# Performance work log

Measured on AMD Instinct MI355X. Metric: run time of the kernel, lower is better.

The kernel has to match this reference:

```python
import jax, jax.numpy as jnp
import numpy as np

N, K, D = 1000000, 8, 32


def setup_inputs() -> dict:
    key = jax.random.key(0)
    k_x, k_mu, k_phi = jax.random.split(key, 3)
    X = jax.random.normal(k_x, (N, D), dtype=jnp.float32)
    # Gaussian.__init__: mu = (rand(dims) - 0.5) * 2, sigma = eye(dims)
    mus = (jax.random.uniform(k_mu, (K, D), dtype=jnp.float32) - 0.5) * 2.0
    sigmas = jnp.broadcast_to(jnp.eye(D, dtype=jnp.float32), (K, D, D)).copy()
    # GMM.__init__: phi ~ Dirichlet(1/count); approximate with normalized uniforms
    phi_raw = jax.random.uniform(k_phi, (K,), dtype=jnp.float32) + 1e-3
    phis = phi_raw / phi_raw.sum()
    return {"X": X, "mus": mus, "sigmas": sigmas, "phis": phis}


def reference(X, mus, sigmas, phis):
    # X: [N, D], mus: [K, D], sigmas: [K, D, D], phis: [K]
    d = X.shape[1]
    inv_sigma = jnp.linalg.pinv(sigmas)                      # [K, D, D]
    _, logdet = jnp.linalg.slogdet(sigmas)                   # [K]
    log_two_pi_dims = d * jnp.log(jnp.asarray(2.0 * np.pi, dtype=X.dtype))
    log_den = 0.5 * (log_two_pi_dims + logdet)               # [K]
    diff = X[:, None, :] - mus[None, :, :]                   # [N, K, D]
    # batched Mahalanobis quadratic form: -0.5 * diff @ inv_sigma @ diff^T (diag)
    quad = -0.5 * jnp.einsum('nkd,kde,nke->nk', diff, inv_sigma, diff)  # [N, K]
    # original subtracts exp(log_den), then scales by phi per mixture
    aff = phis[None, :] * (quad - jnp.exp(log_den)[None, :])  # [N, K]
    # ExpNormalizer.exp_norm == row-wise softmax
    return jax.nn.softmax(aff, axis=1)
```

## Files before the change

### kernel.cpp

```cpp
#include <hip/hip_runtime.h>
#include <hip/hip_bf16.h>
#include <math.h>

#define DDIM 32
#define KMIX 8
#define TPW 10

typedef short bf16x8 __attribute__((ext_vector_type(8)));
typedef float f32x4 __attribute__((ext_vector_type(4)));

__device__ __forceinline__ ushort to_bf16_rne(float f) {
    unsigned u = __builtin_bit_cast(unsigned, f);
    u = (u + 0x7FFFu + ((u >> 16) & 1u)) >> 16;
    return (ushort)u;
}

__global__ __launch_bounds__(512) void gmm_prep(
    const float* __restrict__ S, const float* __restrict__ mus,
    const float* __restrict__ phis, ushort* __restrict__ Wtg,
    ushort* __restrict__ Upan, float* __restrict__ pa2, float* __restrict__ pc)
{
    __shared__ float aug[DDIM][2 * DDIM + 2];
    __shared__ float pivsave[DDIM];
    __shared__ float irts[DDIM];
    __shared__ float wv[DDIM];
    const int k = blockIdx.x;
    const int t = threadIdx.x;
    const int r = t >> 4;
    const int c4 = t & 15;

    aug[r][c4]      = S[k * 1024 + r * 32 + c4];
    aug[r][c4 + 16] = S[k * 1024 + r * 32 + c4 + 16];
    aug[r][c4 + 32] = (c4 == r) ? 1.f : 0.f;
    aug[r][c4 + 48] = (c4 + 16 == r) ? 1.f : 0.f;
    __syncthreads();

    for (int p = 0; p < DDIM; ++p) {
        const float piv = aug[p][p];
        const float f   = aug[r][p];
        const float pr0 = aug[p][c4];
        const float pr1 = aug[p][c4 + 16];
        const float pr2 = aug[p][c4 + 32];
        const float pr3 = aug[p][c4 + 48];
        __syncthreads();
        if (r > p) {
            const float fi = f * __builtin_amdgcn_rcpf(piv);
            aug[r][c4]      = fmaf(-fi, pr0, aug[r][c4]);
            aug[r][c4 + 16] = fmaf(-fi, pr1, aug[r][c4 + 16]);
            aug[r][c4 + 32] = fmaf(-fi, pr2, aug[r][c4 + 32]);
            aug[r][c4 + 48] = fmaf(-fi, pr3, aug[r][c4 + 48]);
        }
        if (t == (p << 4)) pivsave[p] = piv;
        __syncthreads();
    }

    if (t < DDIM) irts[t] = rsqrtf(pivsave[t]);
    __syncthreads();

    if (t < DDIM) {
        float acc = 0.f;
        for (int d = 0; d <= t; ++d)
            acc = fmaf(aug[t][32 + d], mus[k * 32 + d], acc);
        wv[t] = acc * irts[t];
    }
    __syncthreads();

    if (t < DDIM) {
        float acc = 0.f;
        for (int e = t; e < DDIM; ++e)
            acc = fmaf(aug[e][32 + t] * irts[e], wv[e], acc);
        Upan[k * 32 + t] = to_bf16_rne(phis[k] * 1.4426950408889634f * acc);
    }
    if (k == 0 && t >= 256) Upan[t] = 0;

    {
        const int lane0 = (t >> 3) & 63, j0 = t & 7;
        const int d0 = (lane0 >> 4) * 8 + j0;
        const int e0 = lane0 & 15;
        const int e1 = 16 + e0;
        const float f0 = (d0 <= e0) ? aug[e0][32 + d0] * irts[e0] : 0.f;
        const float f1 = (d0 <= e1) ? aug[e1][32 + d0] * irts[e1] : 0.f;
        Wtg[k * 1024 + t]       = to_bf16_rne(f0);
        Wtg[k * 1024 + 512 + t] = to_bf16_rne(f1);
    }

    if (t < 64) {
        float l  = (t < DDIM) ? logf(pivsave[t]) : 0.f;
        float w2 = (t < DDIM) ? wv[t] * wv[t] : 0.f;
        for (int off = 32; off; off >>= 1) {
            l  += __shfl_xor(l, off, 64);
            w2 += __shfl_xor(w2, off, 64);
        }
        if (t == 0) {
            const float eld = expf(0.5f * (DDIM * 1.8378770664093453f + l));
            const float LOG2E = 1.4426950408889634f;
            pa2[k] = -0.5f * phis[k] * LOG2E;
            pc[k]  = (-0.5f * phis[k] * w2 - phis[k] * eld) * LOG2E;
        }
    }
}

template <int CTRL>
__device__ __forceinline__ float dpp_add(float v) {
    int t = __builtin_amdgcn_update_dpp(0, __builtin_bit_cast(int, v), CTRL, 0xF, 0xF, true);
    return v + __builtin_bit_cast(float, t);
}
__device__ __forceinline__ float sel4(float a0, float a1, float a2, float a3, int r) {
    float b0 = (r & 1) ? a1 : a0;
    float b1 = (r & 1) ? a3 : a2;
    return (r & 2) ? b1 : b0;
}
__device__ __forceinline__ float bperm_f(int addr, float v) {
    return __builtin_bit_cast(float, __builtin_amdgcn_ds_bpermute(addr, __builtin_bit_cast(int, v)));
}

__global__ __launch_bounds__(256, 6) void gmm_main(
    const float* __restrict__ X, const ushort* __restrict__ Wtg,
    const ushort* __restrict__ Upan, const float* __restrict__ pa2g,
    const float* __restrict__ pcg, float* __restrict__ out, int N)
{
    __shared__ ushort wtab[KMIX * 1024];
    const int tid = threadIdx.x;
    const int lane = tid & 63;
    const int wid = tid >> 6;
    const int g = lane >> 4;
    const int c = lane & 15;
    const int rsel = c & 3;
    const int r1 = g * 4 + rsel;
    const int p = c >> 2;

    {
        const float4* src = (const float4*)Wtg;
        float4* dst = (float4*)wtab;
#pragma unroll
        for (int i = 0; i < 4; ++i) dst[tid + 256 * i] = src[tid + 256 * i];
    }

    const bf16x8 uf = *(const bf16x8*)(Upan + c * 32 + g * 8);
    float pcv0 = pcg[0], pcv1 = pcg[1], pcv2 = pcg[2], pcv3 = pcg[3];
    float pcv4 = pcg[4], pcv5 = pcg[5], pcv6 = pcg[6], pcv7 = pcg[7];
    const float m8 = fmaxf(fmaxf(fmaxf(pcv0, pcv1), fmaxf(pcv2, pcv3)),
                           fmaxf(fmaxf(pcv4, pcv5), fmaxf(pcv6, pcv7)));
    const float paA = pa2g[2 * p], paB = pa2g[2 * p + 1];
    const float pcsA = pcg[2 * p] - m8, pcsB = pcg[2 * p + 1] - m8;
    const int src_byte = (((p >> 1) * 16 + r1) << 2);

    const int ntiles = N >> 4;
    const int tile0 = (blockIdx.x * 4 + wid) * TPW;
    const float* lp = X + (size_t)tile0 * 512 + c * 32 + g * 8;
    float* op = out + (size_t)(tile0 * 16 + r1) * 8 + p * 2;

    const f32x4 zro = {0.f, 0.f, 0.f, 0.f};
    float4 a0 = {0,0,0,0}, a1 = {0,0,0,0};
    if (tile0 < ntiles) { a0 = *(const float4*)lp; a1 = *(const float4*)(lp + 4); }

    __syncthreads();

#pragma unroll
    for (int it = 0; it < TPW; ++it) {
        const int tile = tile0 + it;
        float4 b0 = a0, b1 = a1;
        if (it + 1 < TPW && tile + 1 < ntiles) {
            b0 = *(const float4*)(lp + 512);
            b1 = *(const float4*)(lp + 516);
        }
        if (tile < ntiles) {
            int4 xi;
            xi.x = __builtin_amdgcn_perm(__builtin_bit_cast(unsigned, a0.y), __builtin_bit_cast(unsigned, a0.x), 0x07060302u);
            xi.y = __builtin_amdgcn_perm(__builtin_bit_cast(unsigned, a0.w), __builtin_bit_cast(unsigned, a0.z), 0x07060302u);
            xi.z = __builtin_amdgcn_perm(__builtin_bit_cast(unsigned, a1.y), __builtin_bit_cast(unsigned, a1.x), 0x07060302u);
            xi.w = __builtin_amdgcn_perm(__builtin_bit_cast(unsigned, a1.w), __builtin_bit_cast(unsigned, a1.z), 0x07060302u);
            const bf16x8 xf = __builtin_bit_cast(bf16x8, xi);

            const f32x4 lin = __builtin_amdgcn_mfma_f32_16x16x32_bf16(uf, xf, zro, 0, 0, 0);

            int la = lane * 16;
            asm volatile("" : "+v"(la));
            const char* wb = (const char*)wtab + la;

            float qa = 0.f, qb = 0.f;
#pragma unroll
            for (int k = 0; k < KMIX; ++k) {
                bf16x8 wf0k = {0, 0, 0, 0, 0, 0, 0, 0};
                if (lane < 32)
                    wf0k = *(const bf16x8*)(wb + (k * 2 + 0) * 1024);
                const bf16x8 wf1k = *(const bf16x8*)(wb + (k * 2 + 1) * 1024);
                f32x4 acc0 = __builtin_amdgcn_mfma_f32_16x16x32_bf16(xf, wf0k, zro, 0, 0, 0);
                f32x4 acc1 = __builtin_amdgcn_mfma_f32_16x16x32_bf16(xf, wf1k, zro, 0, 0, 0);
                float p0 = fmaf(acc1[0], acc1[0], acc0[0] * acc0[0]);
                float p1 = fmaf(acc1[1], acc1[1], acc0[1] * acc0[1]);
                float p2 = fmaf(acc1[2], acc1[2], acc0[2] * acc0[2]);
                float p3 = fmaf(acc1[3], acc1[3], acc0[3] * acc0[3]);
                p0 = dpp_add<0xB1>(p0); p0 = dpp_add<0x4E>(p0);
                p1 = dpp_add<0xB1>(p1); p1 = dpp_add<0x4E>(p1);
                p2 = dpp_add<0xB1>(p2); p2 = dpp_add<0x4E>(p2);
                p3 = dpp_add<0xB1>(p3); p3 = dpp_add<0x4E>(p3);
                float v = sel4(p0, p1, p2, p3, rsel);
                v = dpp_add<0x124>(v);
                v = dpp_add<0x128>(v);
                if ((k >> 1) == 0) { if (p == 0) { if (k & 1) qb = v; else qa = v; } }
                if ((k >> 1) == 1) { if (p == 1) { if (k & 1) qb = v; else qa = v; } }
                if ((k >> 1) == 2) { if (p == 2) { if (k & 1) qb = v; else qa = v; } }
                if ((k >> 1) == 3) { if (p == 3) { if (k & 1) qb = v; else qa = v; } }
            }

            const float l0 = bperm_f(src_byte, lin[0]);
            const float l1 = bperm_f(src_byte, lin[1]);
            const float l2 = bperm_f(src_byte, lin[2]);
            const float l3 = bperm_f(src_byte, lin[3]);
            const float lina = (p & 1) ? l2 : l0;
            const float linb = (p & 1) ? l3 : l1;
            const float aka = fmaf(paA, qa, pcsA) + lina;
            const float akb = fmaf(paB, qb, pcsB) + linb;

            const float ea = __builtin_amdgcn_exp2f(aka);
            const float eb = __builtin_amdgcn_exp2f(akb);
            float s = ea + eb;
            s = dpp_add<0x124>(s); s = dpp_add<0x128>(s);
            const float inv = __builtin_amdgcn_rcpf(s);
            *(float2*)op = make_float2(ea * inv, eb * inv);
        }
        a0 = b0; a1 = b1;
        lp += 512;
        op += 128;
    }
}

extern "C" void kernel_launch(void* const* d_in, const int* in_sizes, int n_in,
                              void* d_out, int out_size, void* d_ws, size_t ws_size,
                              hipStream_t stream) {
    const float* X    = (const float*)d_in[0];
    const float* mus  = (const float*)d_in[1];
    const float* sig  = (const float*)d_in[2];
    const float* phis = (const float*)d_in[3];
    float* out = (float*)d_out;

    float* ws    = (float*)d_ws;
    float* pa2   = ws;
    float* pc    = ws + 8;
    ushort* Upan = (ushort*)(ws + 16);
    ushort* Wtg  = (ushort*)(ws + 272);

    const int N = in_sizes[0] / DDIM;
    const int ntiles = N >> 4;

    gmm_prep<<<KMIX, 512, 0, stream>>>(sig, mus, phis, Wtg, Upan, pa2, pc);

    const int grid = (ntiles + 4 * TPW - 1) / (4 * TPW);
    gmm_main<<<grid, 256, 0, stream>>>(X, Wtg, Upan, pa2, pc, out, N);
}
```

Baseline: 53.50 us.

## Rewrite covariance prep as single-wavefront register elimination using readlane

The prep kernel now runs Gaussian elimination in one 64-lane wavefront instead of 512 threads. Each lane holds one column of the augmented matrix in registers, and pivot values are broadcast with readlane. This removes the two block-wide barriers per pivot step across 32 steps. The cost is serial per-lane work, high register use, and a dynamic select to pick out the pivot row. The main kernel is unchanged, so any gain is limited to the small prep launch that runs before it.

```diff
diff --git a/kernel.cpp b/kernel.cpp
--- a/kernel.cpp
+++ b/kernel.cpp
@@ -14,89 +14,89 @@
     u = (u + 0x7FFFu + ((u >> 16) & 1u)) >> 16;
     return (ushort)u;
 }
-
-__global__ __launch_bounds__(512) void gmm_prep(
+__device__ __forceinline__ float rdlane_f(float v, int sl) {
+    return __builtin_bit_cast(float, __builtin_amdgcn_readlane(__builtin_bit_cast(int, v), sl));
+}
+
+__global__ __launch_bounds__(64) void gmm_prep(
     const float* __restrict__ S, const float* __restrict__ mus,
     const float* __restrict__ phis, ushort* __restrict__ Wtg,
     ushort* __restrict__ Upan, float* __restrict__ pa2, float* __restrict__ pc)
 {
-    __shared__ float aug[DDIM][2 * DDIM + 2];
-    __shared__ float pivsave[DDIM];
-    __shared__ float irts[DDIM];
-    __shared__ float wv[DDIM];
+    __shared__ float lds[DDIM][2 * DDIM + 2];
+    __shared__ float wv_l[DDIM], irt_l[DDIM], mu_l[DDIM];
     const int k = blockIdx.x;
-    const int t = threadIdx.x;
-    const int r = t >> 4;
-    const int c4 = t & 15;
-
-    aug[r][c4]      = S[k * 1024 + r * 32 + c4];
-    aug[r][c4 + 16] = S[k * 1024 + r * 32 + c4 + 16];
-    aug[r][c4 + 32] = (c4 == r) ? 1.f : 0.f;
-    aug[r][c4 + 48] = (c4 + 16 == r) ? 1.f : 0.f;
-    __syncthreads();
-
+    const int l = threadIdx.x;
+
+    float col[DDIM];
+    if (l < DDIM) {
+#pragma unroll
+        for (int r = 0; r < DDIM; ++r) col[r] = S[k * 1024 + r * 32 + l];
+    } else {
+#pragma unroll
+        for (int r = 0; r < DDIM; ++r) col[r] = ((l - DDIM) == r) ? 1.f : 0.f;
+    }
+    if (l < DDIM) mu_l[l] = mus[k * 32 + l];
+
+    float ldet = 0.f;
     for (int p = 0; p < DDIM; ++p) {
-        const float piv = aug[p][p];
-        const float f   = aug[r][p];
-        const float pr0 = aug[p][c4];
-        const float pr1 = aug[p][c4 + 16];
-        const float pr2 = aug[p][c4 + 32];
-        const float pr3 = aug[p][c4 + 48];
-        __syncthreads();
-        if (r > p) {
-            const float fi = f * __builtin_amdgcn_rcpf(piv);
-            aug[r][c4]      = fmaf(-fi, pr0, aug[r][c4]);
-            aug[r][c4 + 16] = fmaf(-fi, pr1, aug[r][c4 + 16]);
-            aug[r][c4 + 32] = fmaf(-fi, pr2, aug[r][c4 + 32]);
-            aug[r][c4 + 48] = fmaf(-fi, pr3, aug[r][c4 + 48]);
-        }
-        if (t == (p << 4)) pivsave[p] = piv;
-        __syncthreads();
-    }
-
-    if (t < DDIM) irts[t] = rsqrtf(pivsave[t]);
-    __syncthreads();
-
-    if (t < DDIM) {
+        float prow = col[0];
+#pragma unroll
+        for (int rr = 1; rr < DDIM; ++rr) prow = (rr == p) ? col[rr] : prow;
+        const float piv = rdlane_f(prow, p);
+        const float rcpp = __builtin_amdgcn_rcpf(piv);
+        ldet += logf(piv);
+#pragma unroll
+        for (int rr = 0; rr < DDIM; ++rr) {
+            const float f = rdlane_f(col[rr], p);
+            const float fi = (rr > p) ? f * rcpp : 0.f;
+            col[rr] = fmaf(-fi, prow, col[rr]);
+        }
+    }
+
+#pragma unroll
+    for (int r = 0; r < DDIM; ++r) lds[r][l] = col[r];
+    __syncthreads();
+
+    if (l < DDIM) irt_l[l] = rsqrtf(lds[l][l]);
+    __syncthreads();
+
+    if (l < DDIM) {
         float acc = 0.f;
-        for (int d = 0; d <= t; ++d)
-            acc = fmaf(aug[t][32 + d], mus[k * 32 + d], acc);
-        wv[t] = acc * irts[t];
-    }
-    __syncthreads();
-
-    if (t < DDIM) {
+        for (int d = 0; d <= l; ++d) acc = fmaf(lds[l][32 + d], mu_l[d], acc);
+        wv_l[l] = acc * irt_l[l];
+    }
+    __syncthreads();
+
+    if (l < DDIM) {
         float acc = 0.f;
-        for (int e = t; e < DDIM; ++e)
-            acc = fmaf(aug[e][32 + t] * irts[e], wv[e], acc);
-        Upan[k * 32 + t] = to_bf16_rne(phis[k] * 1.4426950408889634f * acc);
-    }
-    if (k == 0 && t >= 256) Upan[t] = 0;
-
-    {
-        const int lane0 = (t >> 3) & 63, j0 = t & 7;
-        const int d0 = (lane0 >> 4) * 8 + j0;
-        const int e0 = lane0 & 15;
-        const int e1 = 16 + e0;
-        const float f0 = (d0 <= e0) ? aug[e0][32 + d0] * irts[e0] : 0.f;
-        const float f1 = (d0 <= e1) ? aug[e1][32 + d0] * irts[e1] : 0.f;
-        Wtg[k * 1024 + t]       = to_bf16_rne(f0);
-        Wtg[k * 1024 + 512 + t] = to_bf16_rne(f1);
-    }
-
-    if (t < 64) {
-        float l  = (t < DDIM) ? logf(pivsave[t]) : 0.f;
-        float w2 = (t < DDIM) ? wv[t] * wv[t] : 0.f;
-        for (int off = 32; off; off >>= 1) {
-            l  += __shfl_xor(l, off, 64);
-            w2 += __shfl_xor(w2, off, 64);
-        }
-        if (t == 0) {
-            const float eld = expf(0.5f * (DDIM * 1.8378770664093453f + l));
-            const float LOG2E = 1.4426950408889634f;
-            pa2[k] = -0.5f * phis[k] * LOG2E;
-            pc[k]  = (-0.5f * phis[k] * w2 - phis[k] * eld) * LOG2E;
-        }
+        for (int e = l; e < DDIM; ++e)
+            acc = fmaf(lds[e][32 + l] * irt_l[e], wv_l[e], acc);
+        Upan[k * 32 + l] = to_bf16_rne(phis[k] * 1.4426950408889634f * acc);
+    }
+    if (k == 0)
+        for (int i = l; i < 256; i += 64) Upan[256 + i] = 0;
+
+#pragma unroll
+    for (int h = 0; h < 2; ++h) {
+        ushort tmp[8];
+#pragma unroll
+        for (int j = 0; j < 8; ++j) {
+            const int d = (l >> 4) * 8 + j;
+            const int e = h * 16 + (l & 15);
+            const float fv = (d <= e) ? lds[e][32 + d] * irt_l[e] : 0.f;
+            tmp[j] = to_bf16_rne(fv);
+        }
+        *(bf16x8*)(Wtg + k * 1024 + h * 512 + l * 8) = *(const bf16x8*)tmp;
+    }
+
+    if (l == 0) {
+        float w2 = 0.f;
+        for (int e = 0; e < DDIM; ++e) w2 = fmaf(wv_l[e], wv_l[e], w2);
+        const float eld = expf(0.5f * (DDIM * 1.8378770664093453f + ldet));
+        const float LOG2E = 1.4426950408889634f;
+        pa2[k] = -0.5f * phis[k] * LOG2E;
+        pc[k]  = (-0.5f * phis[k] * w2 - phis[k] * eld) * LOG2E;
     }
 }
 
@@ -244,7 +244,7 @@
     const int N = in_sizes[0] / DDIM;
     const int ntiles = N >> 4;
 
-    gmm_prep<<<KMIX, 512, 0, stream>>>(sig, mus, phis, Wtg, Upan, pa2, pc);
+    gmm_prep<<<KMIX, 64, 0, stream>>>(sig, mus, phis, Wtg, Upan, pa2, pc);
 
     const int grid = (ntiles + 4 * TPW - 1) / (4 * TPW);
     gmm_main<<<grid, 256, 0, stream>>>(X, Wtg, Upan, pa2, pc, out, N);
```

Result: slower. 65.26 us (+22.0%).
